# Kernel optimization log

Hardware: AMD Instinct MI355X
Metric: run time of the kernel (lower is better)

Reference implementation:

```python
import jax, jax.numpy as jnp
import numpy as np

N_NODES = 100000
N_EDGES = 1600000
N_GRAPHS = 512
X_DIM = 4
H = 64
L = 3
NUM_CLASS = 3


def setup_inputs() -> dict:
    key = jax.random.key(0)
    ks = jax.random.split(key, 16)
    s = 0.1
    return {
        "x": jax.random.normal(ks[0], (N_NODES, X_DIM), jnp.float32),
        "edge_index": jax.random.randint(ks[1], (2, N_EDGES), 0, N_NODES, jnp.int64),
        "batch": jnp.sort(jax.random.randint(ks[2], (N_NODES,), 0, N_GRAPHS, jnp.int64)),
        "edge_attr": jax.random.uniform(ks[3], (N_EDGES,), jnp.float32),
        # node embedding
        "W_emb": jax.random.normal(ks[4], (X_DIM, H), jnp.float32) * s,
        "b_emb": jnp.zeros((H,), jnp.float32),
        # LEConv per-layer params (stacked over layers)
        "W1": jax.random.normal(ks[5], (L, H, H), jnp.float32) * s,
        "b1": jnp.zeros((L, H), jnp.float32),
        "W2": jax.random.normal(ks[6], (L, H, H), jnp.float32) * s,  # no bias (lin2)
        "W3": jax.random.normal(ks[7], (L, H, H), jnp.float32) * s,
        "b3": jnp.zeros((L, H), jnp.float32),
        # fc_out head
        "Wf1": jax.random.normal(ks[8], (H, 2 * H), jnp.float32) * s,
        "bf1": jnp.zeros((2 * H,), jnp.float32),
        "Wf2": jax.random.normal(ks[9], (2 * H, NUM_CLASS), jnp.float32) * s,
        "bf2": jnp.zeros((NUM_CLASS,), jnp.float32),
    }


def reference(x, edge_index, batch, edge_attr, W_emb, b_emb, W1, b1, W2, W3, b3,
              Wf1, bf1, Wf2, bf2):
    src, dst = edge_index[0], edge_index[1]
    # node embedding
    h = x @ W_emb + b_emb  # [N, H]
    # stacked LEConv layers: x_i' = sum_{j->i} e_ji * (lin1(x_j) - lin2(x_i)) + lin3(x_i)
    for l in range(L):
        a = h @ W1[l] + b1[l]          # [N, H]
        b = h @ W2[l]                  # [N, H] (lin2 has no bias)
        msg = (a[src] - b[dst]) * edge_attr[:, None]  # [E, H]
        agg = jax.ops.segment_sum(msg, dst, num_segments=N_NODES)
        h = jax.nn.relu(agg + h @ W3[l] + b3[l])
    # global mean pool per graph
    sums = jax.ops.segment_sum(h, batch, num_segments=N_GRAPHS)  # [G, H]
    cnt = jax.ops.segment_sum(jnp.ones((N_NODES,), h.dtype), batch, num_segments=N_GRAPHS)
    graph_x = sums / jnp.maximum(cnt, 1.0)[:, None]
    # fc_out head
    hid = jax.nn.relu(graph_x @ Wf1 + bf1)
    return hid @ Wf2 + bf2  # [G, NUM_CLASS]
```

## Files before the change

kernel.cpp:

```cpp
#include <hip/hip_runtime.h>

#define N_NODES 100000
#define N_EDGES 1600000
#define N_GRAPHS 512
#define X_DIM 4
#define H 64
#define LAYERS 3
#define NUM_CLASS 3
#define NBLK 256
#define EPB (N_EDGES / NBLK)
#define BKT_BITS 9
#define BKT_SZ 512
#define NBKT ((N_NODES + BKT_SZ - 1) / BKT_SZ)
#define MHIST (NBKT * NBLK)
#define LROW 72
#define NCHUNKS ((N_NODES + 63) / 64)

typedef unsigned short ushort;
typedef short bf16x8 __attribute__((ext_vector_type(8)));
typedef unsigned short ush8 __attribute__((ext_vector_type(8)));
typedef float floatx4 __attribute__((ext_vector_type(4)));

__device__ __forceinline__ ushort f2bf(float v) {
    unsigned u = __float_as_uint(v);
    unsigned r = (u + 0x7fff + ((u >> 16) & 1)) >> 16;
    return (ushort)r;
}
__device__ __forceinline__ float bf2f(ushort s) {
    return __uint_as_float(((unsigned)s) << 16);
}

__global__ void embed_kernel(const float* __restrict__ x, const float* __restrict__ Wemb,
                             const float* __restrict__ bemb, ushort* __restrict__ h) {
    int i = blockIdx.x * blockDim.x + threadIdx.x;
    if (i >= N_NODES * H) return;
    int n = i >> 6, f = i & 63;
    float acc = bemb[f];
#pragma unroll
    for (int k = 0; k < X_DIM; ++k)
        acc += x[n * X_DIM + k] * Wemb[k * H + f];
    h[i] = f2bf(acc);
}

__global__ __launch_bounds__(256) void hist1_kernel(const int* __restrict__ dst,
                                                    int* __restrict__ histM) {
    __shared__ int hist[NBKT];
    int t = threadIdx.x, b = blockIdx.x;
    for (int i = t; i < NBKT; i += 256) hist[i] = 0;
    __syncthreads();
    int e0 = b * EPB;
    for (int j = t; j < EPB; j += 256) {
        int d = dst[e0 + j];
        atomicAdd(hist + (d >> BKT_BITS), 1);
    }
    __syncthreads();
    for (int i = t; i < NBKT; i += 256) histM[i * NBLK + b] = hist[i];
}

__global__ __launch_bounds__(512) void gscan1_kernel(const int* __restrict__ v,
                                                     int* __restrict__ incl,
                                                     int* __restrict__ partials) {
    __shared__ int s[512];
    int tid = threadIdx.x;
    int i = blockIdx.x * 512 + tid;
    int x = (i < MHIST) ? v[i] : 0;
    s[tid] = x;
    for (int off = 1; off < 512; off <<= 1) {
        __syncthreads();
        int tv = (tid >= off) ? s[tid - off] : 0;
        __syncthreads();
        s[tid] += tv;
    }
    __syncthreads();
    if (i < MHIST) incl[i] = s[tid];
    if (tid == 511) partials[blockIdx.x] = s[tid];
}

__global__ __launch_bounds__(512) void gscan2_kernel(const int* __restrict__ partials,
                                                     int* __restrict__ chunk_off, int nchunk) {
    __shared__ int s[512];
    int tid = threadIdx.x;
    s[tid] = (tid < nchunk) ? partials[tid] : 0;
    for (int off = 1; off < 512; off <<= 1) {
        __syncthreads();
        int tv = (tid >= off) ? s[tid - off] : 0;
        __syncthreads();
        s[tid] += tv;
    }
    __syncthreads();
    int excl = (tid == 0) ? 0 : s[tid - 1];
    __syncthreads();
    if (tid < nchunk) chunk_off[tid] = excl;
}

__global__ void gscan3_kernel(const int* __restrict__ v, const int* __restrict__ incl,
                              const int* __restrict__ chunk_off,
                              int* __restrict__ ebase, int* __restrict__ bkt_ptr) {
    int i = blockIdx.x * 256 + threadIdx.x;
    if (i >= MHIST) return;
    int e = incl[i] + chunk_off[i >> 9] - v[i];
    ebase[i] = e;
    if ((i & (NBLK - 1)) == 0) bkt_ptr[i / NBLK] = e;
    if (i == MHIST - 1) bkt_ptr[NBKT] = e + v[i];
}

__global__ __launch_bounds__(256) void scatter1_kernel(
    const int* __restrict__ src, const int* __restrict__ dst, const float* __restrict__ ea,
    const int* __restrict__ ebase, unsigned* __restrict__ eb_se, int* __restrict__ eb_dst) {
    __shared__ int cur[NBKT];
    int t = threadIdx.x, b = blockIdx.x;
    for (int i = t; i < NBKT; i += 256) cur[i] = ebase[i * NBLK + b];
    __syncthreads();
    int e0 = b * EPB;
    for (int j = t; j < EPB; j += 256) {
        int e = e0 + j;
        int d = dst[e];
        int k = d >> BKT_BITS;
        int pos = atomicAdd(cur + k, 1);
        eb_se[pos] = ((unsigned)src[e] << 15) | (unsigned)f2bf(ea[e]);
        eb_dst[pos] = d;
    }
}

__global__ __launch_bounds__(512) void bucket_kernel(
    const int* __restrict__ bkt_ptr, const unsigned* __restrict__ eb_se,
    const int* __restrict__ eb_dst,
    int* __restrict__ row_ptr, float* __restrict__ degw, unsigned* __restrict__ epack) {
    __shared__ int cnt[BKT_SZ];
    __shared__ float dws[BKT_SZ];
    __shared__ int s[BKT_SZ];
    __shared__ int cur[BKT_SZ];
    int k = blockIdx.x, t = threadIdx.x;
    int base = k << BKT_BITS;
    int nn = N_NODES - base;
    if (nn > BKT_SZ) nn = BKT_SZ;
    cnt[t] = 0;
    dws[t] = 0.0f;
    __syncthreads();
    int beg = bkt_ptr[k], end = bkt_ptr[k + 1];
    for (int j = beg + t; j < end; j += 512) {
        int d = eb_dst[j] - base;
        atomicAdd(cnt + d, 1);
        atomicAdd(dws + d, __uint_as_float((eb_se[j] & 0x7FFFu) << 16));
    }
    __syncthreads();
    s[t] = cnt[t];
    for (int off = 1; off < 512; off <<= 1) {
        __syncthreads();
        int tv = (t >= off) ? s[t - off] : 0;
        __syncthreads();
        s[t] += tv;
    }
    __syncthreads();
    int rstart = beg + s[t] - cnt[t];
    if (t < nn) {
        row_ptr[base + t] = rstart;
        degw[base + t] = dws[t];
        cur[t] = rstart;
    }
    __syncthreads();
    for (int j = beg + t; j < end; j += 512) {
        unsigned se = eb_se[j];
        int d = eb_dst[j] - base;
        int pos = atomicAdd(cur + d, 1);
        epack[pos] = se;
    }
    if (k == NBKT - 1 && t == 0) row_ptr[N_NODES] = N_EDGES;
}

__global__ __launch_bounds__(256) void linAB_kernel(
    const ushort* __restrict__ h, const float* __restrict__ degw,
    const float* __restrict__ W1, const float* __restrict__ bias1,
    const float* __restrict__ W2, const float* __restrict__ W3,
    const float* __restrict__ bias3,
    ushort* __restrict__ a, ushort* __restrict__ aggb) {
    __shared__ alignas(16) ushort ah[64 * LROW];
    int t = threadIdx.x;
    int wv = t >> 6, lane = t & 63;
    int quad = lane >> 4, m16 = lane & 15;
    int f = wv * 16 + m16;
    bf16x8 B[3][2][2];
    const float* Ws[3] = {W1, W2, W3};
#pragma unroll
    for (int wsel = 0; wsel < 3; ++wsel) {
#pragma unroll
        for (int kh = 0; kh < 2; ++kh) {
#pragma unroll
            for (int j = 0; j < 8; ++j) {
                float w = Ws[wsel][(kh * 32 + quad * 8 + j) * H + f];
                ushort hi = f2bf(w);
                B[wsel][kh][0][j] = (short)hi;
                B[wsel][kh][1][j] = (short)f2bf(w - bf2f(hi));
            }
        }
    }
    float bb1 = bias1[f], bb3 = bias3[f];
    for (int chunk = blockIdx.x; chunk < NCHUNKS; chunk += gridDim.x) {
        int nbase = chunk * 64;
        __syncthreads();
        for (int v = t; v < 64 * 8; v += 256) {
            int nl = v >> 3, k0 = (v & 7) * 8;
            int n = nbase + nl;
            ush8 val = {0, 0, 0, 0, 0, 0, 0, 0};
            if (n < N_NODES) val = *(const ush8*)&h[(size_t)n * H + k0];
            *(ush8*)&ah[nl * LROW + k0] = val;
        }
        __syncthreads();
#pragma unroll
        for (int ng = 0; ng < 4; ++ng) {
            int abase = (ng * 16 + m16) * LROW + quad * 8;
            bf16x8 A0 = *(const bf16x8*)&ah[abase];
            bf16x8 A1 = *(const bf16x8*)&ah[abase + 32];
            floatx4 acc1 = {0.f, 0.f, 0.f, 0.f};
            floatx4 acc2 = {0.f, 0.f, 0.f, 0.f};
            floatx4 acc3 = {0.f, 0.f, 0.f, 0.f};
            acc1 = __builtin_amdgcn_mfma_f32_16x16x32_bf16(A0, B[0][0][0], acc1, 0, 0, 0);
            acc1 = __builtin_amdgcn_mfma_f32_16x16x32_bf16(A0, B[0][0][1], acc1, 0, 0, 0);
            acc1 = __builtin_amdgcn_mfma_f32_16x16x32_bf16(A1, B[0][1][0], acc1, 0, 0, 0);
            acc1 = __builtin_amdgcn_mfma_f32_16x16x32_bf16(A1, B[0][1][1], acc1, 0, 0, 0);
            acc2 = __builtin_amdgcn_mfma_f32_16x16x32_bf16(A0, B[1][0][0], acc2, 0, 0, 0);
            acc2 = __builtin_amdgcn_mfma_f32_16x16x32_bf16(A0, B[1][0][1], acc2, 0, 0, 0);
            acc2 = __builtin_amdgcn_mfma_f32_16x16x32_bf16(A1, B[1][1][0], acc2, 0, 0, 0);
            acc2 = __builtin_amdgcn_mfma_f32_16x16x32_bf16(A1, B[1][1][1], acc2, 0, 0, 0);
            acc3 = __builtin_amdgcn_mfma_f32_16x16x32_bf16(A0, B[2][0][0], acc3, 0, 0, 0);
            acc3 = __builtin_amdgcn_mfma_f32_16x16x32_bf16(A0, B[2][0][1], acc3, 0, 0, 0);
            acc3 = __builtin_amdgcn_mfma_f32_16x16x32_bf16(A1, B[2][1][0], acc3, 0, 0, 0);
            acc3 = __builtin_amdgcn_mfma_f32_16x16x32_bf16(A1, B[2][1][1], acc3, 0, 0, 0);
            int nrow = nbase + ng * 16 + quad * 4;
#pragma unroll
            for (int r = 0; r < 4; ++r) {
                int n = nrow + r;
                if (n < N_NODES) {
                    float dw = degw[n];
                    a[(size_t)n * H + f] = f2bf(acc1[r] + bb1);
                    aggb[(size_t)n * H + f] = f2bf(acc3[r] + bb3 - acc2[r] * dw);
                }
            }
        }
    }
}

__global__ __launch_bounds__(256) void gather_kernel(
    const int* __restrict__ row_ptr, const unsigned* __restrict__ epack,
    const ushort* __restrict__ a, const ushort* __restrict__ aggb,
    ushort* __restrict__ h) {
    int n = blockIdx.x * 4 + (threadIdx.x >> 6);
    if (n >= N_NODES) return;
    int lane = threadIdx.x & 63;
    int q = lane >> 3, s = lane & 7;
    int beg = row_ptr[n], end = row_ptr[n + 1];
    float acc[8] = {0.f, 0.f, 0.f, 0.f, 0.f, 0.f, 0.f, 0.f};
    for (int j = beg; j < end; j += 32) {
        unsigned w[4];
#pragma unroll
        for (int k = 0; k < 4; ++k) {
            int jk = j + k * 8 + q;
            w[k] = (jk < end) ? epack[jk] : 0u;
        }
        ush8 av[4];
#pragma unroll
        for (int k = 0; k < 4; ++k)
            av[k] = *(const ush8*)&a[(size_t)(w[k] >> 15) * H + s * 8];
#pragma unroll
        for (int k = 0; k < 4; ++k) {
            float e = __uint_as_float((w[k] & 0x7FFFu) << 16);
#pragma unroll
            for (int i = 0; i < 8; ++i)
                acc[i] += e * bf2f((ushort)av[k][i]);
        }
    }
#pragma unroll
    for (int i = 0; i < 8; ++i) {
        acc[i] += __shfl_xor(acc[i], 8);
        acc[i] += __shfl_xor(acc[i], 16);
        acc[i] += __shfl_xor(acc[i], 32);
    }
    if (q == 0) {
        ush8 ag = *(const ush8*)&aggb[(size_t)n * H + s * 8];
        ush8 r;
#pragma unroll
        for (int i = 0; i < 8; ++i)
            r[i] = (short)f2bf(fmaxf(acc[i] + bf2f((ushort)ag[i]), 0.0f));
        *(ush8*)&h[(size_t)n * H + s * 8] = r;
    }
}

__device__ __forceinline__ int lower_bound(const int* __restrict__ arr, int n, int key) {
    int lo = 0, hi = n;
    while (lo < hi) {
        int mid = (lo + hi) >> 1;
        if (arr[mid] < key) lo = mid + 1; else hi = mid;
    }
    return lo;
}

__global__ __launch_bounds__(256) void poolhead_kernel(
    const ushort* __restrict__ h, const int* __restrict__ batch,
    const float* __restrict__ Wf1, const float* __restrict__ bf1v,
    const float* __restrict__ Wf2, const float* __restrict__ bf2v,
    float* __restrict__ out) {
    __shared__ float psum[4][H];
    __shared__ float gx[H];
    __shared__ float hid[2 * H];
    int g = blockIdx.x, t = threadIdx.x;
    int s = lower_bound(batch, N_NODES, g);
    int e = lower_bound(batch, N_NODES, g + 1);
    int lane = t & 63, wv = t >> 6;
    int o = lane & 7;
    int nd = t >> 3;
    float acc[8] = {0.f, 0.f, 0.f, 0.f, 0.f, 0.f, 0.f, 0.f};
    for (int n = s + nd; n < e; n += 32) {
        ush8 v = *(const ush8*)&h[(size_t)n * H + o * 8];
#pragma unroll
        for (int i = 0; i < 8; ++i) acc[i] += bf2f((ushort)v[i]);
    }
#pragma unroll
    for (int i = 0; i < 8; ++i) {
        acc[i] += __shfl_xor(acc[i], 8);
        acc[i] += __shfl_xor(acc[i], 16);
        acc[i] += __shfl_xor(acc[i], 32);
    }
    if (lane < 8) {
#pragma unroll
        for (int i = 0; i < 8; ++i) psum[wv][o * 8 + i] = acc[i];
    }
    __syncthreads();
    if (t < H) {
        float c = (float)(e - s);
        gx[t] = (psum[0][t] + psum[1][t] + psum[2][t] + psum[3][t]) / fmaxf(c, 1.0f);
    }
    __syncthreads();
    if (t < 2 * H) {
        float acc2 = bf1v[t];
        for (int k = 0; k < H; ++k) acc2 += gx[k] * Wf1[k * 2 * H + t];
        hid[t] = fmaxf(acc2, 0.0f);
    }
    __syncthreads();
    if (t < NUM_CLASS) {
        float o2 = bf2v[t];
        for (int k = 0; k < 2 * H; ++k) o2 += hid[k] * Wf2[k * NUM_CLASS + t];
        out[g * NUM_CLASS + t] = o2;
    }
}

extern "C" void kernel_launch(void* const* d_in, const int* in_sizes, int n_in,
                              void* d_out, int out_size, void* d_ws, size_t ws_size,
                              hipStream_t stream) {
    const float* x    = (const float*)d_in[0];
    const int*  ei    = (const int*)d_in[1];
    const int*  batch = (const int*)d_in[2];
    const float* ea   = (const float*)d_in[3];
    const float* Wemb = (const float*)d_in[4];
    const float* bemb = (const float*)d_in[5];
    const float* pW1  = (const float*)d_in[6];
    const float* pb1  = (const float*)d_in[7];
    const float* pW2  = (const float*)d_in[8];
    const float* pW3  = (const float*)d_in[9];
    const float* pb3  = (const float*)d_in[10];
    const float* Wf1  = (const float*)d_in[11];
    const float* bf1v = (const float*)d_in[12];
    const float* Wf2  = (const float*)d_in[13];
    const float* bf2v = (const float*)d_in[14];
    float* out = (float*)d_out;

    const int* src = ei;
    const int* dst = ei + N_EDGES;

    const size_t NH = (size_t)N_NODES * H;
    char* p = (char*)d_ws;
    ushort* h       = (ushort*)p;            p += NH * 2;
    ushort* a       = (ushort*)p;            p += NH * 2;
    ushort* aggb    = (ushort*)p;            p += NH * 2;
    unsigned* epack = (unsigned*)p;          p += (size_t)N_EDGES * 4;
    int*   histM    = (int*)p;               p += MHIST * 4;
    int*   incl     = (int*)p;               p += MHIST * 4;
    int*   ebase    = (int*)p;               p += MHIST * 4;
    int*   partials = (int*)p;               p += 512 * 4;
    int*   chunk_off= (int*)p;               p += 512 * 4;
    int*   bkt_ptr  = (int*)p;               p += (NBKT + 1) * 4;
    int*   row_ptr  = (int*)p;               p += (N_NODES + 1) * 4;
    float* degw     = (float*)p;             p += N_NODES * 4;
    unsigned* eb_se = (unsigned*)a;
    int*     eb_dst = (int*)aggb;

    hist1_kernel<<<NBLK, 256, 0, stream>>>(dst, histM);
    gscan1_kernel<<<MHIST / 512, 512, 0, stream>>>(histM, incl, partials);
    gscan2_kernel<<<1, 512, 0, stream>>>(partials, chunk_off, MHIST / 512);
    gscan3_kernel<<<(MHIST + 255) / 256, 256, 0, stream>>>(histM, incl, chunk_off, ebase, bkt_ptr);
    scatter1_kernel<<<NBLK, 256, 0, stream>>>(src, dst, ea, ebase, eb_se, eb_dst);
    bucket_kernel<<<NBKT, 512, 0, stream>>>(bkt_ptr, eb_se, eb_dst, row_ptr, degw, epack);

    embed_kernel<<<(N_NODES * H + 255) / 256, 256, 0, stream>>>(x, Wemb, bemb, h);

    for (int l = 0; l < LAYERS; ++l) {
        linAB_kernel<<<512, 256, 0, stream>>>(
            h, degw,
            pW1 + (size_t)l * H * H, pb1 + (size_t)l * H,
            pW2 + (size_t)l * H * H,
            pW3 + (size_t)l * H * H, pb3 + (size_t)l * H,
            a, aggb);
        gather_kernel<<<(N_NODES + 3) / 4, 256, 0, stream>>>(row_ptr, epack, a, aggb, h);
    }

    poolhead_kernel<<<N_GRAPHS, 256, 0, stream>>>(h, batch, Wf1, bf1v, Wf2, bf2v, out);
}
```

Before: 358.1 us.

## Aggregate before transform and fold embedding into layer-one weights

Reorders each LEConv layer to aggregate edge-weighted neighbor features first and then apply the linear maps (sum e*W1 h = W1 sum e*h), so the gather reads h directly and a single fused kernel does all three matmuls plus ReLU. For layer one, the embedding is folded into precomputed 4xH weight products, so the gather only touches the 4-dim raw x per edge instead of 64-dim features. This removes one full edge gather over 64-wide features and the embed pass. In exchange it adds small precompute, xgather and combine kernels and changes where bf16 rounding happens, since the aggregated message is stored in bf16 before the matmul.

```diff
diff --git a/kernel.cpp b/kernel.cpp
--- a/kernel.cpp
+++ b/kernel.cpp
@@ -30,16 +30,27 @@
     return __uint_as_float(((unsigned)s) << 16);
 }
 
-__global__ void embed_kernel(const float* __restrict__ x, const float* __restrict__ Wemb,
-                             const float* __restrict__ bemb, ushort* __restrict__ h) {
-    int i = blockIdx.x * blockDim.x + threadIdx.x;
-    if (i >= N_NODES * H) return;
-    int n = i >> 6, f = i & 63;
-    float acc = bemb[f];
-#pragma unroll
-    for (int k = 0; k < X_DIM; ++k)
-        acc += x[n * X_DIM + k] * Wemb[k * H + f];
-    h[i] = f2bf(acc);
+__global__ void precomp_kernel(const float* __restrict__ Wemb, const float* __restrict__ bemb,
+                               const float* __restrict__ W1, const float* __restrict__ b1,
+                               const float* __restrict__ W2, const float* __restrict__ W3,
+                               const float* __restrict__ b3,
+                               float* __restrict__ G, float* __restrict__ C) {
+    int f = threadIdx.x;
+    if (f >= H) return;
+    const float* Ws[3] = {W1, W2, W3};
+#pragma unroll
+    for (int wsel = 0; wsel < 3; ++wsel) {
+        const float* W = Ws[wsel];
+#pragma unroll
+        for (int c = 0; c < X_DIM; ++c) {
+            float g = 0.f;
+            for (int k = 0; k < H; ++k) g += Wemb[c * H + k] * W[k * H + f];
+            G[wsel * 256 + c * H + f] = g;
+        }
+        float cb = (wsel == 0) ? b1[f] : (wsel == 2) ? b3[f] : 0.f;
+        for (int k = 0; k < H; ++k) cb += bemb[k] * W[k * H + f];
+        C[wsel * H + f] = cb;
+    }
 }
 
 __global__ __launch_bounds__(256) void hist1_kernel(const int* __restrict__ dst,
@@ -168,82 +179,54 @@
     if (k == NBKT - 1 && t == 0) row_ptr[N_NODES] = N_EDGES;
 }
 
-__global__ __launch_bounds__(256) void linAB_kernel(
-    const ushort* __restrict__ h, const float* __restrict__ degw,
-    const float* __restrict__ W1, const float* __restrict__ bias1,
-    const float* __restrict__ W2, const float* __restrict__ W3,
-    const float* __restrict__ bias3,
-    ushort* __restrict__ a, ushort* __restrict__ aggb) {
-    __shared__ alignas(16) ushort ah[64 * LROW];
-    int t = threadIdx.x;
-    int wv = t >> 6, lane = t & 63;
-    int quad = lane >> 4, m16 = lane & 15;
-    int f = wv * 16 + m16;
-    bf16x8 B[3][2][2];
-    const float* Ws[3] = {W1, W2, W3};
-#pragma unroll
-    for (int wsel = 0; wsel < 3; ++wsel) {
-#pragma unroll
-        for (int kh = 0; kh < 2; ++kh) {
-#pragma unroll
-            for (int j = 0; j < 8; ++j) {
-                float w = Ws[wsel][(kh * 32 + quad * 8 + j) * H + f];
-                ushort hi = f2bf(w);
-                B[wsel][kh][0][j] = (short)hi;
-                B[wsel][kh][1][j] = (short)f2bf(w - bf2f(hi));
-            }
-        }
-    }
-    float bb1 = bias1[f], bb3 = bias3[f];
-    for (int chunk = blockIdx.x; chunk < NCHUNKS; chunk += gridDim.x) {
-        int nbase = chunk * 64;
-        __syncthreads();
-        for (int v = t; v < 64 * 8; v += 256) {
-            int nl = v >> 3, k0 = (v & 7) * 8;
-            int n = nbase + nl;
-            ush8 val = {0, 0, 0, 0, 0, 0, 0, 0};
-            if (n < N_NODES) val = *(const ush8*)&h[(size_t)n * H + k0];
-            *(ush8*)&ah[nl * LROW + k0] = val;
-        }
-        __syncthreads();
-#pragma unroll
-        for (int ng = 0; ng < 4; ++ng) {
-            int abase = (ng * 16 + m16) * LROW + quad * 8;
-            bf16x8 A0 = *(const bf16x8*)&ah[abase];
-            bf16x8 A1 = *(const bf16x8*)&ah[abase + 32];
-            floatx4 acc1 = {0.f, 0.f, 0.f, 0.f};
-            floatx4 acc2 = {0.f, 0.f, 0.f, 0.f};
-            floatx4 acc3 = {0.f, 0.f, 0.f, 0.f};
-            acc1 = __builtin_amdgcn_mfma_f32_16x16x32_bf16(A0, B[0][0][0], acc1, 0, 0, 0);
-            acc1 = __builtin_amdgcn_mfma_f32_16x16x32_bf16(A0, B[0][0][1], acc1, 0, 0, 0);
-            acc1 = __builtin_amdgcn_mfma_f32_16x16x32_bf16(A1, B[0][1][0], acc1, 0, 0, 0);
-            acc1 = __builtin_amdgcn_mfma_f32_16x16x32_bf16(A1, B[0][1][1], acc1, 0, 0, 0);
-            acc2 = __builtin_amdgcn_mfma_f32_16x16x32_bf16(A0, B[1][0][0], acc2, 0, 0, 0);
-            acc2 = __builtin_amdgcn_mfma_f32_16x16x32_bf16(A0, B[1][0][1], acc2, 0, 0, 0);
-            acc2 = __builtin_amdgcn_mfma_f32_16x16x32_bf16(A1, B[1][1][0], acc2, 0, 0, 0);
-            acc2 = __builtin_amdgcn_mfma_f32_16x16x32_bf16(A1, B[1][1][1], acc2, 0, 0, 0);
-            acc3 = __builtin_amdgcn_mfma_f32_16x16x32_bf16(A0, B[2][0][0], acc3, 0, 0, 0);
-            acc3 = __builtin_amdgcn_mfma_f32_16x16x32_bf16(A0, B[2][0][1], acc3, 0, 0, 0);
-            acc3 = __builtin_amdgcn_mfma_f32_16x16x32_bf16(A1, B[2][1][0], acc3, 0, 0, 0);
-            acc3 = __builtin_amdgcn_mfma_f32_16x16x32_bf16(A1, B[2][1][1], acc3, 0, 0, 0);
-            int nrow = nbase + ng * 16 + quad * 4;
-#pragma unroll
-            for (int r = 0; r < 4; ++r) {
-                int n = nrow + r;
-                if (n < N_NODES) {
-                    float dw = degw[n];
-                    a[(size_t)n * H + f] = f2bf(acc1[r] + bb1);
-                    aggb[(size_t)n * H + f] = f2bf(acc3[r] + bb3 - acc2[r] * dw);
-                }
-            }
-        }
-    }
+__global__ __launch_bounds__(256) void xgather_kernel(
+    const int* __restrict__ row_ptr, const unsigned* __restrict__ epack,
+    const float* __restrict__ x, float* __restrict__ mx) {
+    int n = blockIdx.x * 4 + (threadIdx.x >> 6);
+    if (n >= N_NODES) return;
+    int lane = threadIdx.x & 63;
+    int q = lane >> 1, cp = lane & 1;
+    int beg = row_ptr[n], end = row_ptr[n + 1];
+    float a0 = 0.f, a1 = 0.f;
+    for (int j = beg; j < end; j += 32) {
+        int jk = j + q;
+        unsigned w = (jk < end) ? epack[jk] : 0u;
+        float2 xv = *(const float2*)&x[(size_t)(w >> 15) * X_DIM + cp * 2];
+        float e = __uint_as_float((w & 0x7FFFu) << 16);
+        a0 += e * xv.x;
+        a1 += e * xv.y;
+    }
+#pragma unroll
+    for (int mask = 2; mask <= 32; mask <<= 1) {
+        a0 += __shfl_xor(a0, mask);
+        a1 += __shfl_xor(a1, mask);
+    }
+    if (lane < 2) {
+        mx[(size_t)n * X_DIM + lane * 2] = a0;
+        mx[(size_t)n * X_DIM + lane * 2 + 1] = a1;
+    }
+}
+
+__global__ void combine_kernel(const float* __restrict__ x, const float* __restrict__ mx,
+                               const float* __restrict__ degw,
+                               const float* __restrict__ G, const float* __restrict__ C,
+                               ushort* __restrict__ h) {
+    int i = blockIdx.x * blockDim.x + threadIdx.x;
+    if (i >= N_NODES * H) return;
+    int n = i >> 6, f = i & 63;
+    floatx4 xv = *(const floatx4*)&x[(size_t)n * X_DIM];
+    floatx4 mv = *(const floatx4*)&mx[(size_t)n * X_DIM];
+    float dw = degw[n];
+    float t1 = mv[0] * G[f] + mv[1] * G[64 + f] + mv[2] * G[128 + f] + mv[3] * G[192 + f];
+    float t2 = xv[0] * G[256 + f] + xv[1] * G[320 + f] + xv[2] * G[384 + f] + xv[3] * G[448 + f];
+    float t3 = xv[0] * G[512 + f] + xv[1] * G[576 + f] + xv[2] * G[640 + f] + xv[3] * G[704 + f];
+    float v = t1 + dw * C[f] + t3 + C[128 + f] - (t2 + C[64 + f]) * dw;
+    h[i] = f2bf(fmaxf(v, 0.0f));
 }
 
 __global__ __launch_bounds__(256) void gather_kernel(
     const int* __restrict__ row_ptr, const unsigned* __restrict__ epack,
-    const ushort* __restrict__ a, const ushort* __restrict__ aggb,
-    ushort* __restrict__ h) {
+    const ushort* __restrict__ h, ushort* __restrict__ m) {
     int n = blockIdx.x * 4 + (threadIdx.x >> 6);
     if (n >= N_NODES) return;
     int lane = threadIdx.x & 63;
@@ -260,7 +243,7 @@
         ush8 av[4];
 #pragma unroll
         for (int k = 0; k < 4; ++k)
-            av[k] = *(const ush8*)&a[(size_t)(w[k] >> 15) * H + s * 8];
+            av[k] = *(const ush8*)&h[(size_t)(w[k] >> 15) * H + s * 8];
 #pragma unroll
         for (int k = 0; k < 4; ++k) {
             float e = __uint_as_float((w[k] & 0x7FFFu) << 16);
@@ -276,12 +259,90 @@
         acc[i] += __shfl_xor(acc[i], 32);
     }
     if (q == 0) {
-        ush8 ag = *(const ush8*)&aggb[(size_t)n * H + s * 8];
         ush8 r;
 #pragma unroll
-        for (int i = 0; i < 8; ++i)
-            r[i] = (short)f2bf(fmaxf(acc[i] + bf2f((ushort)ag[i]), 0.0f));
-        *(ush8*)&h[(size_t)n * H + s * 8] = r;
+        for (int i = 0; i < 8; ++i) r[i] = (short)f2bf(acc[i]);
+        *(ush8*)&m[(size_t)n * H + s * 8] = r;
+    }
+}
+
+__global__ __launch_bounds__(256) void linC_kernel(
+    ushort* __restrict__ h, const ushort* __restrict__ m,
+    const float* __restrict__ degw,
+    const float* __restrict__ W1, const float* __restrict__ bias1,
+    const float* __restrict__ W2, const float* __restrict__ W3,
+    const float* __restrict__ bias3) {
+    __shared__ alignas(16) ushort ah[64 * LROW];
+    __shared__ alignas(16) ushort am[64 * LROW];
+    int t = threadIdx.x;
+    int wv = t >> 6, lane = t & 63;
+    int quad = lane >> 4, m16 = lane & 15;
+    int f = wv * 16 + m16;
+    bf16x8 B[3][2][2];
+    const float* Ws[3] = {W1, W2, W3};
+#pragma unroll
+    for (int wsel = 0; wsel < 3; ++wsel) {
+#pragma unroll
+        for (int kh = 0; kh < 2; ++kh) {
+#pragma unroll
+            for (int j = 0; j < 8; ++j) {
+                float w = Ws[wsel][(kh * 32 + quad * 8 + j) * H + f];
+                ushort hi = f2bf(w);
+                B[wsel][kh][0][j] = (short)hi;
+                B[wsel][kh][1][j] = (short)f2bf(w - bf2f(hi));
+            }
+        }
+    }
+    float bb1 = bias1[f], bb3 = bias3[f];
+    for (int chunk = blockIdx.x; chunk < NCHUNKS; chunk += gridDim.x) {
+        int nbase = chunk * 64;
+        __syncthreads();
+        for (int v = t; v < 64 * 8; v += 256) {
+            int nl = v >> 3, k0 = (v & 7) * 8;
+            int n = nbase + nl;
+            ush8 vh = {0, 0, 0, 0, 0, 0, 0, 0};
+            ush8 vm = {0, 0, 0, 0, 0, 0, 0, 0};
+            if (n < N_NODES) {
+                vh = *(const ush8*)&h[(size_t)n * H + k0];
+                vm = *(const ush8*)&m[(size_t)n * H + k0];
+            }
+            *(ush8*)&ah[nl * LROW + k0] = vh;
+            *(ush8*)&am[nl * LROW + k0] = vm;
+        }
+        __syncthreads();
+#pragma unroll
+        for (int ng = 0; ng < 4; ++ng) {
+            int abase = (ng * 16 + m16) * LROW + quad * 8;
+            bf16x8 Ah0 = *(const bf16x8*)&ah[abase];
+            bf16x8 Ah1 = *(const bf16x8*)&ah[abase + 32];
+            bf16x8 Am0 = *(const bf16x8*)&am[abase];
+            bf16x8 Am1 = *(const bf16x8*)&am[abase + 32];
+            floatx4 acc1 = {0.f, 0.f, 0.f, 0.f};
+            floatx4 acc2 = {0.f, 0.f, 0.f, 0.f};
+            floatx4 acc3 = {0.f, 0.f, 0.f, 0.f};
+            acc1 = __builtin_amdgcn_mfma_f32_16x16x32_bf16(Am0, B[0][0][0], acc1, 0, 0, 0);
+            acc1 = __builtin_amdgcn_mfma_f32_16x16x32_bf16(Am0, B[0][0][1], acc1, 0, 0, 0);
+            acc1 = __builtin_amdgcn_mfma_f32_16x16x32_bf16(Am1, B[0][1][0], acc1, 0, 0, 0);
+            acc1 = __builtin_amdgcn_mfma_f32_16x16x32_bf16(Am1, B[0][1][1], acc1, 0, 0, 0);
+            acc2 = __builtin_amdgcn_mfma_f32_16x16x32_bf16(Ah0, B[1][0][0], acc2, 0, 0, 0);
+            acc2 = __builtin_amdgcn_mfma_f32_16x16x32_bf16(Ah0, B[1][0][1], acc2, 0, 0, 0);
+            acc2 = __builtin_amdgcn_mfma_f32_16x16x32_bf16(Ah1, B[1][1][0], acc2, 0, 0, 0);
+            acc2 = __builtin_amdgcn_mfma_f32_16x16x32_bf16(Ah1, B[1][1][1], acc2, 0, 0, 0);
+            acc3 = __builtin_amdgcn_mfma_f32_16x16x32_bf16(Ah0, B[2][0][0], acc3, 0, 0, 0);
+            acc3 = __builtin_amdgcn_mfma_f32_16x16x32_bf16(Ah0, B[2][0][1], acc3, 0, 0, 0);
+            acc3 = __builtin_amdgcn_mfma_f32_16x16x32_bf16(Ah1, B[2][1][0], acc3, 0, 0, 0);
+            acc3 = __builtin_amdgcn_mfma_f32_16x16x32_bf16(Ah1, B[2][1][1], acc3, 0, 0, 0);
+            int nrow = nbase + ng * 16 + quad * 4;
+#pragma unroll
+            for (int r = 0; r < 4; ++r) {
+                int n = nrow + r;
+                if (n < N_NODES) {
+                    float dw = degw[n];
+                    float v = acc1[r] + dw * bb1 + acc3[r] + bb3 - acc2[r] * dw;
+                    h[(size_t)n * H + f] = f2bf(fmaxf(v, 0.0f));
+                }
+            }
+        }
     }
 }
 
@@ -369,8 +430,8 @@
     const size_t NH = (size_t)N_NODES * H;
     char* p = (char*)d_ws;
     ushort* h       = (ushort*)p;            p += NH * 2;
-    ushort* a       = (ushort*)p;            p += NH * 2;
-    ushort* aggb    = (ushort*)p;            p += NH * 2;
+    ushort* m       = (ushort*)p;            p += NH * 2;
+    float*  mx      = (float*)p;             p += (size_t)N_NODES * X_DIM * 4;
     unsigned* epack = (unsigned*)p;          p += (size_t)N_EDGES * 4;
     int*   histM    = (int*)p;               p += MHIST * 4;
     int*   incl     = (int*)p;               p += MHIST * 4;
@@ -380,8 +441,12 @@
     int*   bkt_ptr  = (int*)p;               p += (NBKT + 1) * 4;
     int*   row_ptr  = (int*)p;               p += (N_NODES + 1) * 4;
     float* degw     = (float*)p;             p += N_NODES * 4;
-    unsigned* eb_se = (unsigned*)a;
-    int*     eb_dst = (int*)aggb;
+    float* Gbuf     = (float*)p;             p += 3 * 256 * 4;
+    float* Cbuf     = (float*)p;             p += 3 * 64 * 4;
+    unsigned* eb_se = (unsigned*)m;
+    int*     eb_dst = (int*)h;
+
+    precomp_kernel<<<1, 64, 0, stream>>>(Wemb, bemb, pW1, pb1, pW2, pW3, pb3, Gbuf, Cbuf);
 
     hist1_kernel<<<NBLK, 256, 0, stream>>>(dst, histM);
     gscan1_kernel<<<MHIST / 512, 512, 0, stream>>>(histM, incl, partials);
@@ -390,16 +455,16 @@
     scatter1_kernel<<<NBLK, 256, 0, stream>>>(src, dst, ea, ebase, eb_se, eb_dst);
     bucket_kernel<<<NBKT, 512, 0, stream>>>(bkt_ptr, eb_se, eb_dst, row_ptr, degw, epack);
 
-    embed_kernel<<<(N_NODES * H + 255) / 256, 256, 0, stream>>>(x, Wemb, bemb, h);
-
-    for (int l = 0; l < LAYERS; ++l) {
-        linAB_kernel<<<512, 256, 0, stream>>>(
-            h, degw,
+    xgather_kernel<<<(N_NODES + 3) / 4, 256, 0, stream>>>(row_ptr, epack, x, mx);
+    combine_kernel<<<(N_NODES * H + 255) / 256, 256, 0, stream>>>(x, mx, degw, Gbuf, Cbuf, h);
+
+    for (int l = 1; l < LAYERS; ++l) {
+        gather_kernel<<<(N_NODES + 3) / 4, 256, 0, stream>>>(row_ptr, epack, h, m);
+        linC_kernel<<<512, 256, 0, stream>>>(
+            h, m, degw,
             pW1 + (size_t)l * H * H, pb1 + (size_t)l * H,
             pW2 + (size_t)l * H * H,
-            pW3 + (size_t)l * H * H, pb3 + (size_t)l * H,
-            a, aggb);
-        gather_kernel<<<(N_NODES + 3) / 4, 256, 0, stream>>>(row_ptr, epack, a, aggb, h);
+            pW3 + (size_t)l * H * H, pb3 + (size_t)l * H);
     }
 
     poolhead_kernel<<<N_GRAPHS, 256, 0, stream>>>(h, batch, Wf1, bf1v, Wf2, bf2v, out);
```

Result: faster. 331.9 us (-7.3%).
